# Kernel tuning notes

Hardware: AMD Instinct MI355X
Metric: run time of the kernel (lower is better)

Reference implementation:

```python
import jax, jax.numpy as jnp
import numpy as np

B, S, D, H = 2, 1024, 1024, 16
DK = D // H  # 64, per-head dim; quaternion component dim = DK // 4 = 16
NEG = -1e9


def qlinear(x, wr, wi, wj, wk, b):
    """Quaternion linear layer: Hamilton product x (x) W, per-component weights (D/4, D/4)."""
    xr, xi, xj, xk = jnp.split(x, 4, axis=-1)
    o_r = xr @ wr - xi @ wi - xj @ wj - xk @ wk
    o_i = xr @ wi + xi @ wr + xj @ wk - xk @ wj
    o_j = xr @ wj - xi @ wk + xj @ wr + xk @ wi
    o_k = xr @ wk + xi @ wj - xj @ wi + xk @ wr
    return jnp.concatenate([o_r, o_i, o_j, o_k], axis=-1) + b


def quat_scores(q, k):
    """Hamilton product q (x) k^T over chunked head dim. q,k: [B,H,S,DK]."""
    ar, ax, ay, az = jnp.split(q, 4, axis=-1)
    br, bx, by, bz = jnp.split(k, 4, axis=-1)
    mm = lambda a, b: jnp.einsum('bhsd,bhtd->bhst', a, b)
    r = mm(ar, br) - mm(ax, bx) - mm(ay, by) - mm(az, bz)
    i = mm(ar, bx) + mm(ax, br) + mm(ay, bz) - mm(az, by)
    j = mm(ar, by) - mm(ax, bz) + mm(ay, br) + mm(az, bx)
    kk = mm(ar, bz) + mm(ax, by) - mm(ay, bx) + mm(az, br)
    return r, i, j, kk


def quat_mix(sr, si, sj, sk, v):
    """Hamilton product scores (x) v (no transpose). s*: [B,H,S,S], v: [B,H,S,DK]."""
    br, bx, by, bz = jnp.split(v, 4, axis=-1)
    mm = lambda a, b: jnp.einsum('bhst,bhtd->bhsd', a, b)
    r = mm(sr, br) - mm(si, bx) - mm(sj, by) - mm(sk, bz)
    i = mm(sr, bx) + mm(si, br) + mm(sj, bz) - mm(sk, by)
    j = mm(sr, by) - mm(si, bz) + mm(sj, br) + mm(sk, bx)
    k = mm(sr, bz) + mm(si, by) - mm(sj, bx) + mm(sk, br)
    return jnp.concatenate([r, i, j, k], axis=-1)


def mha_forward(q, k, v, mask,
                wq_r, wq_i, wq_j, wq_k, bq,
                wk_r, wk_i, wk_j, wk_k, bk,
                wv_r, wv_i, wv_j, wv_k, bv,
                wo_r, wo_i, wo_j, wo_k, bo):
    bs = q.shape[0]
    def heads(x):
        return x.reshape(bs, -1, H, DK).transpose(0, 2, 1, 3)  # [B,H,S,DK]
    qh = heads(qlinear(q, wq_r, wq_i, wq_j, wq_k, bq))
    kh = heads(qlinear(k, wk_r, wk_i, wk_j, wk_k, bk))
    vh = heads(qlinear(v, wv_r, wv_i, wv_j, wv_k, bv))
    scale = 1.0 / jnp.sqrt(jnp.asarray(DK, qh.dtype))
    sr, si, sj, sk = [s * scale for s in quat_scores(qh, kh)]
    m = (mask[:, None] != 0)  # [B,1,1,S] broadcast over [B,H,S,S]
    sm = lambda s: jax.nn.softmax(jnp.where(m, s, NEG), axis=-1)
    out = quat_mix(sm(sr), sm(si), sm(sj), sm(sk), vh)  # [B,H,S,DK]
    concat = out.transpose(0, 2, 1, 3).reshape(bs, -1, D)
    return qlinear(concat, wo_r, wo_i, wo_j, wo_k, bo)


def setup_inputs() -> dict:
    key = jax.random.key(0)
    ks = jax.random.split(key, 24)
    dq = D // 4
    w_scale = 1.0 / np.sqrt(dq)
    inp = {
        'q': jax.random.normal(ks[0], (B, S, D), jnp.float32),
        'k': jax.random.normal(ks[1], (B, S, D), jnp.float32),
        'v': jax.random.normal(ks[2], (B, S, D), jnp.float32),
        'mask': jnp.ones((B, 1, S), jnp.int32),
    }
    names = ['wq_r', 'wq_i', 'wq_j', 'wq_k', 'wk_r', 'wk_i', 'wk_j', 'wk_k',
             'wv_r', 'wv_i', 'wv_j', 'wv_k', 'wo_r', 'wo_i', 'wo_j', 'wo_k']
    for n, kk in zip(names, ks[3:19]):
        inp[n] = jax.random.normal(kk, (dq, dq), jnp.float32) * w_scale
    for n, kk in zip(['bq', 'bk', 'bv', 'bo'], ks[19:23]):
        inp[n] = jax.random.normal(kk, (D,), jnp.float32) * 0.01
    return inp


def reference(q, k, v, mask,
              wq_r, wq_i, wq_j, wq_k, bq,
              wk_r, wk_i, wk_j, wk_k, bk,
              wv_r, wv_i, wv_j, wv_k, bv,
              wo_r, wo_i, wo_j, wo_k, bo):
    return mha_forward(q, k, v, mask,
                       wq_r, wq_i, wq_j, wq_k, bq,
                       wk_r, wk_i, wk_j, wk_k, bk,
                       wv_r, wv_i, wv_j, wv_k, bv,
                       wo_r, wo_i, wo_j, wo_k, bo)
```

## Files before the change

kernel.cpp:

```cpp
#include <hip/hip_runtime.h>

#define LOG2E 1.4426950408889634f
#define SC2   0.18033688011112042f

typedef short s16x8 __attribute__((ext_vector_type(8)));
typedef short s16x4 __attribute__((ext_vector_type(4)));
typedef float f32x4 __attribute__((ext_vector_type(4)));
typedef unsigned int u32x4 __attribute__((ext_vector_type(4)));

static __device__ __forceinline__ unsigned short f2bf(float f) {
  return __builtin_bit_cast(unsigned short, (__bf16)f);
}

static __device__ __forceinline__ void gload_lds16(const void* g, void* l) {
  __builtin_amdgcn_global_load_lds(
      (__attribute__((address_space(1))) void*)g,
      (__attribute__((address_space(3))) void*)l, 16, 0, 0);
}

__global__ void k_f2b(const float* __restrict__ a, const float* __restrict__ b,
                      const float* __restrict__ c, unsigned short* __restrict__ oa,
                      unsigned short* __restrict__ ob, unsigned short* __restrict__ oc) {
  const int z = blockIdx.y;
  const float* in = z == 0 ? a : z == 1 ? b : c;
  unsigned short* out = z == 0 ? oa : z == 1 ? ob : oc;
  int i = blockIdx.x * blockDim.x + threadIdx.x;
  const float4 v = ((const float4*)in)[i];
  ushort4 o;
  o.x = f2bf(v.x); o.y = f2bf(v.y); o.z = f2bf(v.z); o.w = f2bf(v.w);
  ((ushort4*)out)[i] = o;
}

struct WArgs {
  const float* w[16];
  unsigned short* dst[4];
};
__global__ void k_build_w(WArgs args) {
  __shared__ float tile[64][65];
  const int z = blockIdx.y;
  const int k0 = (blockIdx.x & 15) * 64, n0 = (blockIdx.x >> 4) * 64;
  const int a = k0 >> 8, c = n0 >> 8;
  const int   selr[16] = {0,1,2,3, 1,0,3,2, 2,3,0,1, 3,2,1,0};
  const float sgnr[16] = {1,1,1,1, -1,1,-1,1, -1,1,1,-1, -1,-1,1,1};
  const float* sp = args.w[z*4 + selr[a*4 + c]];
  const float sg = sgnr[a*4 + c];
  unsigned short* Wt = args.dst[z];
  const int k0l = k0 & 255, n0l = n0 & 255;
  const int rr = threadIdx.x >> 6, cc = threadIdx.x & 63;
#pragma unroll
  for (int p = 0; p < 16; ++p) {
    int r = p*4 + rr;
    tile[r][cc] = sp[(k0l + r)*256 + n0l + cc];
  }
  __syncthreads();
#pragma unroll
  for (int p = 0; p < 16; ++p) {
    int nn = p*4 + rr;
    Wt[(size_t)(n0 + nn)*1024 + k0 + cc] = f2bf(tile[cc][nn] * sg);
  }
}

__global__ __launch_bounds__(256, 2) void k_gemm_qkv(
    const unsigned short* __restrict__ Xq, const unsigned short* __restrict__ Xk,
    const unsigned short* __restrict__ Xv,
    const unsigned short* __restrict__ Wq, const unsigned short* __restrict__ Wk,
    const unsigned short* __restrict__ Wv,
    const float* __restrict__ bq, const float* __restrict__ bk, const float* __restrict__ bv,
    unsigned short* __restrict__ Qp, unsigned short* __restrict__ Kp,
    unsigned short* __restrict__ VpT) {
  __shared__ unsigned short As[2][128*32];
  __shared__ unsigned short Bs[2][128*32];
  const int z = blockIdx.z;
  const unsigned short* A  = z == 0 ? Xq : z == 1 ? Xk : Xv;
  const unsigned short* Bt = z == 0 ? Wq : z == 1 ? Wk : Wv;
  const float* bias        = z == 0 ? bq : z == 1 ? bk : bv;
  const int K = 1024, N = 1024;
  const int tid = threadIdx.x;
  const int lane = tid & 63, wave = tid >> 6;
  const int lo = lane & 15, hi = lane >> 4;
  const int m0 = blockIdx.x * 128, n0 = blockIdx.y * 128;
  const int wr_ = (wave >> 1) * 64, wc_ = (wave & 1) * 64;
  const int e0 = tid*8, e1 = 2048 + tid*8;
  const int r0 = e0 >> 5, c0 = e0 & 31, r1 = e1 >> 5, c1 = e1 & 31;
  f32x4 acc[4][4] = {};

  gload_lds16(A  + (size_t)(m0 + r0)*K + c0, &As[0][e0]);
  gload_lds16(Bt + (size_t)(n0 + r0)*K + c0, &Bs[0][e0]);
  gload_lds16(A  + (size_t)(m0 + r1)*K + c1, &As[0][e1]);
  gload_lds16(Bt + (size_t)(n0 + r1)*K + c1, &Bs[0][e1]);
  __syncthreads();
  int cur = 0;
  for (int k0 = 0; k0 < K; k0 += 32) {
    if (k0 + 32 < K) {
      int kn = k0 + 32;
      gload_lds16(A  + (size_t)(m0 + r0)*K + (kn + c0), &As[cur^1][e0]);
      gload_lds16(Bt + (size_t)(n0 + r0)*K + (kn + c0), &Bs[cur^1][e0]);
      gload_lds16(A  + (size_t)(m0 + r1)*K + (kn + c1), &As[cur^1][e1]);
      gload_lds16(Bt + (size_t)(n0 + r1)*K + (kn + c1), &Bs[cur^1][e1]);
    }
    s16x8 af[4], bfv[4];
#pragma unroll
    for (int mf = 0; mf < 4; ++mf)
      af[mf] = __builtin_bit_cast(s16x8, *(const u32x4*)&As[cur][(wr_ + mf*16 + lo)*32 + hi*8]);
#pragma unroll
    for (int nf = 0; nf < 4; ++nf)
      bfv[nf] = __builtin_bit_cast(s16x8, *(const u32x4*)&Bs[cur][(wc_ + nf*16 + lo)*32 + hi*8]);
#pragma unroll
    for (int mf = 0; mf < 4; ++mf)
#pragma unroll
      for (int nf = 0; nf < 4; ++nf)
        acc[mf][nf] = __builtin_amdgcn_mfma_f32_16x16x32_bf16(af[mf], bfv[nf], acc[mf][nf], 0, 0, 0);
    __syncthreads();
    cur ^= 1;
  }
  if (z < 2) {
    unsigned short* Cout = z == 0 ? Qp : Kp;
#pragma unroll
    for (int nf = 0; nf < 4; ++nf) {
      int col = n0 + wc_ + nf*16 + lo;
      float bv2 = bias[col];
#pragma unroll
      for (int mf = 0; mf < 4; ++mf)
#pragma unroll
        for (int j = 0; j < 4; ++j) {
          int row = m0 + wr_ + mf*16 + hi*4 + j;
          Cout[(size_t)row*N + col] = f2bf(acc[mf][nf][j] + bv2);
        }
    }
  } else {
#pragma unroll
    for (int nf = 0; nf < 4; ++nf) {
      int col = n0 + wc_ + nf*16 + lo;
      float bv2 = bias[col];
      int hh = col >> 6, dk = col & 63;
#pragma unroll
      for (int mf = 0; mf < 4; ++mf) {
        int row = m0 + wr_ + mf*16 + hi*4;
        int bb = row >> 10, t = row & 1023;
        s16x4 pk;
#pragma unroll
        for (int j = 0; j < 4; ++j) pk[j] = (short)f2bf(acc[mf][nf][j] + bv2);
        *(s16x4*)(VpT + ((size_t)((bb*16 + hh)*64 + dk))*1024 + t) = pk;
      }
    }
  }
}

__global__ __launch_bounds__(256, 2) void k_gemm_o(
    const unsigned short* __restrict__ A, const unsigned short* __restrict__ Bt,
    const float* __restrict__ bias, float* __restrict__ Cout) {
  __shared__ unsigned short As[2][128*32];
  __shared__ unsigned short Bs[2][128*32];
  const int K = 1024, N = 1024;
  const int tid = threadIdx.x;
  const int lane = tid & 63, wave = tid >> 6;
  const int lo = lane & 15, hi = lane >> 4;
  const int m0 = blockIdx.x * 128, n0 = blockIdx.y * 128;
  const int wr_ = (wave >> 1) * 64, wc_ = (wave & 1) * 64;
  const int e0 = tid*8, e1 = 2048 + tid*8;
  const int r0 = e0 >> 5, c0 = e0 & 31, r1 = e1 >> 5, c1 = e1 & 31;
  f32x4 acc[4][4] = {};
  gload_lds16(A  + (size_t)(m0 + r0)*K + c0, &As[0][e0]);
  gload_lds16(Bt + (size_t)(n0 + r0)*K + c0, &Bs[0][e0]);
  gload_lds16(A  + (size_t)(m0 + r1)*K + c1, &As[0][e1]);
  gload_lds16(Bt + (size_t)(n0 + r1)*K + c1, &Bs[0][e1]);
  __syncthreads();
  int cur = 0;
  for (int k0 = 0; k0 < K; k0 += 32) {
    if (k0 + 32 < K) {
      int kn = k0 + 32;
      gload_lds16(A  + (size_t)(m0 + r0)*K + (kn + c0), &As[cur^1][e0]);
      gload_lds16(Bt + (size_t)(n0 + r0)*K + (kn + c0), &Bs[cur^1][e0]);
      gload_lds16(A  + (size_t)(m0 + r1)*K + (kn + c1), &As[cur^1][e1]);
      gload_lds16(Bt + (size_t)(n0 + r1)*K + (kn + c1), &Bs[cur^1][e1]);
    }
    s16x8 af[4], bfv[4];
#pragma unroll
    for (int mf = 0; mf < 4; ++mf)
      af[mf] = __builtin_bit_cast(s16x8, *(const u32x4*)&As[cur][(wr_ + mf*16 + lo)*32 + hi*8]);
#pragma unroll
    for (int nf = 0; nf < 4; ++nf)
      bfv[nf] = __builtin_bit_cast(s16x8, *(const u32x4*)&Bs[cur][(wc_ + nf*16 + lo)*32 + hi*8]);
#pragma unroll
    for (int mf = 0; mf < 4; ++mf)
#pragma unroll
      for (int nf = 0; nf < 4; ++nf)
        acc[mf][nf] = __builtin_amdgcn_mfma_f32_16x16x32_bf16(af[mf], bfv[nf], acc[mf][nf], 0, 0, 0);
    __syncthreads();
    cur ^= 1;
  }
#pragma unroll
  for (int nf = 0; nf < 4; ++nf) {
    int col = n0 + wc_ + nf*16 + lo;
    float bv2 = bias[col];
#pragma unroll
    for (int mf = 0; mf < 4; ++mf)
#pragma unroll
      for (int j = 0; j < 4; ++j) {
        int row = m0 + wr_ + mf*16 + hi*4 + j;
        Cout[(size_t)row*N + col] = acc[mf][nf][j] + bv2;
      }
  }
}

__global__ __launch_bounds__(256, 2) void k_attn(
    const unsigned short* __restrict__ Qp, const unsigned short* __restrict__ Kp,
    const unsigned short* __restrict__ VpT, const int* __restrict__ mask,
    unsigned short* __restrict__ O) {
  __shared__ float mbias[1024];
  const int bh = blockIdx.x & 31, qb = blockIdx.x >> 5;
  const int b = bh >> 4, h = bh & 15;
  for (int t = threadIdx.x; t < 1024; t += 256)
    mbias[t] = mask[b*1024 + t] ? 0.0f : -2.0e9f;
  __syncthreads();
  const int lane = threadIdx.x & 63, wave = threadIdx.x >> 6;
  const int lo = lane & 15, hi = lane >> 4;
  const int s0 = qb*64 + wave*16;

  const int qsel[16] = {0,1,2,3, 1,0,3,2, 2,3,0,1, 3,2,1,0};
  const int qsgn[16] = {1,-1,-1,-1, 1,1,-1,1, 1,1,1,-1, 1,-1,1,1};
  const int vsgn[16] = {1,1,1,1, -1,1,-1,1, -1,1,1,-1, -1,-1,1,1};

  s16x8 qf[4][2];
  {
    const size_t qoff = ((size_t)(b*1024 + s0 + lo))*1024 + h*64;
    const int ch_hi = hi >> 1, dlo = (hi & 1) * 8;
#pragma unroll
    for (int c = 0; c < 4; ++c)
#pragma unroll
      for (int kb = 0; kb < 2; ++kb) {
        int ch = kb*2 + ch_hi;
        int p = qsel[c*4 + ch];
        u32x4 raw = *(const u32x4*)(Qp + qoff + p*16 + dlo);
        unsigned int mk = (qsgn[c*4 + ch] < 0) ? 0x80008000u : 0u;
        raw ^= mk;
        qf[c][kb] = __builtin_bit_cast(s16x8, raw);
      }
  }

  f32x4 acc[4][4] = {};
  float lsum[4] = {0.f, 0.f, 0.f, 0.f};

  const unsigned short* vtb = VpT + ((size_t)bh*64 + lo)*1024;

  for (int t0 = 0; t0 < 1024; t0 += 32) {
    const size_t koffA = ((size_t)(b*1024 + t0 + lo))*1024 + h*64;
    s16x8 kfA0 = __builtin_bit_cast(s16x8, *(const u32x4*)(Kp + koffA + hi*8));
    s16x8 kfA1 = __builtin_bit_cast(s16x8, *(const u32x4*)(Kp + koffA + 32 + hi*8));
    const size_t koffB = koffA + (size_t)16*1024;
    s16x8 kfB0 = __builtin_bit_cast(s16x8, *(const u32x4*)(Kp + koffB + hi*8));
    s16x8 kfB1 = __builtin_bit_cast(s16x8, *(const u32x4*)(Kp + koffB + 32 + hi*8));
    s16x4 vA[4], vB[4], vAn[4], vBn[4];
#pragma unroll
    for (int g = 0; g < 4; ++g) {
      vA[g] = *(const s16x4*)(vtb + (size_t)g*16*1024 + t0 + hi*4);
      vB[g] = *(const s16x4*)(vtb + (size_t)g*16*1024 + t0 + 16 + hi*4);
    }
    vAn[0] = vA[0]; vBn[0] = vB[0];
#pragma unroll
    for (int g = 1; g < 4; ++g) {
      vAn[g] = vA[g] ^ (short)0x8000;
      vBn[g] = vB[g] ^ (short)0x8000;
    }
    f32x4 mbA = *(const f32x4*)&mbias[t0 + hi*4];
    f32x4 mbB = *(const f32x4*)&mbias[t0 + 16 + hi*4];

#pragma unroll
    for (int c = 0; c < 4; ++c) {
      f32x4 sA = {0.f,0.f,0.f,0.f}, sB = {0.f,0.f,0.f,0.f};
      sA = __builtin_amdgcn_mfma_f32_16x16x32_bf16(kfA0, qf[c][0], sA, 0, 0, 0);
      sA = __builtin_amdgcn_mfma_f32_16x16x32_bf16(kfA1, qf[c][1], sA, 0, 0, 0);
      sB = __builtin_amdgcn_mfma_f32_16x16x32_bf16(kfB0, qf[c][0], sB, 0, 0, 0);
      sB = __builtin_amdgcn_mfma_f32_16x16x32_bf16(kfB1, qf[c][1], sB, 0, 0, 0);
      float p0 = __builtin_exp2f(__builtin_fmaf(sA[0], SC2, mbA[0]));
      float p1 = __builtin_exp2f(__builtin_fmaf(sA[1], SC2, mbA[1]));
      float p2 = __builtin_exp2f(__builtin_fmaf(sA[2], SC2, mbA[2]));
      float p3 = __builtin_exp2f(__builtin_fmaf(sA[3], SC2, mbA[3]));
      float p4 = __builtin_exp2f(__builtin_fmaf(sB[0], SC2, mbB[0]));
      float p5 = __builtin_exp2f(__builtin_fmaf(sB[1], SC2, mbB[1]));
      float p6 = __builtin_exp2f(__builtin_fmaf(sB[2], SC2, mbB[2]));
      float p7 = __builtin_exp2f(__builtin_fmaf(sB[3], SC2, mbB[3]));
      lsum[c] += ((p0 + p1) + (p2 + p3)) + ((p4 + p5) + (p6 + p7));
      s16x4 pfA, pfB;
      pfA[0] = (short)f2bf(p0); pfA[1] = (short)f2bf(p1);
      pfA[2] = (short)f2bf(p2); pfA[3] = (short)f2bf(p3);
      pfB[0] = (short)f2bf(p4); pfB[1] = (short)f2bf(p5);
      pfB[2] = (short)f2bf(p6); pfB[3] = (short)f2bf(p7);
#pragma unroll
      for (int g = 0; g < 4; ++g) {
        int idx = c*4 + g;
        int p = qsel[idx];
        s16x4 va = vsgn[idx] < 0 ? vAn[p] : vA[p];
        s16x4 vb = vsgn[idx] < 0 ? vBn[p] : vB[p];
        acc[c][g] = __builtin_amdgcn_mfma_f32_16x16x16bf16_1k(pfA, va, acc[c][g], 0, 0, 0);
        acc[c][g] = __builtin_amdgcn_mfma_f32_16x16x16bf16_1k(pfB, vb, acc[c][g], 0, 0, 0);
      }
    }
  }
  float rl[4];
#pragma unroll
  for (int c = 0; c < 4; ++c) {
    float l = lsum[c];
    l += __shfl_xor(l, 16);
    l += __shfl_xor(l, 32);
    rl[c] = 1.0f / l;
  }
  const size_t obase = ((size_t)(b*1024 + s0 + hi*4))*1024 + h*64;
#pragma unroll
  for (int j = 0; j < 4; ++j) {
    float r0 = __shfl(rl[0], hi*4 + j);
    float r1 = __shfl(rl[1], hi*4 + j);
    float r2 = __shfl(rl[2], hi*4 + j);
    float r3 = __shfl(rl[3], hi*4 + j);
#pragma unroll
    for (int g = 0; g < 4; ++g) {
      float o = acc[0][g][j]*r0 + acc[1][g][j]*r1 + acc[2][g][j]*r2 + acc[3][g][j]*r3;
      O[obase + (size_t)j*1024 + g*16 + lo] = f2bf(o);
    }
  }
}

extern "C" void kernel_launch(void* const* d_in, const int* in_sizes, int n_in,
                              void* d_out, int out_size, void* d_ws, size_t ws_size,
                              hipStream_t stream) {
  const float* q  = (const float*)d_in[0];
  const float* k  = (const float*)d_in[1];
  const float* v  = (const float*)d_in[2];
  const int* mask = (const int*)d_in[3];
  const float* bq = (const float*)d_in[20];
  const float* bk = (const float*)d_in[21];
  const float* bv = (const float*)d_in[22];
  const float* bo = (const float*)d_in[23];

  unsigned short* ws = (unsigned short*)d_ws;
  unsigned short* Xq = ws;
  unsigned short* Xk = Xq + 2048*1024;
  unsigned short* Xv = Xk + 2048*1024;
  unsigned short* Wq = Xv + 2048*1024;
  unsigned short* Wk = Wq + 1024*1024;
  unsigned short* Wv = Wk + 1024*1024;
  unsigned short* Wo = Wv + 1024*1024;
  unsigned short* Qp = Wo + 1024*1024;
  unsigned short* Kp = Qp + 2048*1024;
  unsigned short* VpT = Kp + 2048*1024;
  unsigned short* Ob = VpT + 2048*1024;

  k_f2b<<<dim3(2048, 3), 256, 0, stream>>>(q, k, v, Xq, Xk, Xv);

  WArgs wa;
  for (int i = 0; i < 16; ++i) wa.w[i] = (const float*)d_in[4 + i];
  wa.dst[0] = Wq; wa.dst[1] = Wk; wa.dst[2] = Wv; wa.dst[3] = Wo;
  k_build_w<<<dim3(256, 4), 256, 0, stream>>>(wa);

  k_gemm_qkv<<<dim3(16, 8, 3), 256, 0, stream>>>(Xq, Xk, Xv, Wq, Wk, Wv,
                                                 bq, bk, bv, Qp, Kp, VpT);
  k_attn<<<512, 256, 0, stream>>>(Qp, Kp, VpT, mask, Ob);
  k_gemm_o<<<dim3(16, 8), 256, 0, stream>>>(Ob, Wo, bo, (float*)d_out);
}
```

Measured before the change: 253.2 us.

## Split attention key range across two blocks and add combine kernel

Attention blocks now each process half of the key sequence, doubling the grid size, and write unnormalized bf16 partial outputs and row sums to workspace. A new combine kernel adds the two partials, normalizes by the summed row sums, and writes the bf16 output. This aims to raise GPU occupancy and parallelism. The cost is an extra launch, extra global memory traffic for the partials, and some bf16 rounding of intermediate accumulators.

```diff
diff --git a/kernel.cpp b/kernel.cpp
--- a/kernel.cpp
+++ b/kernel.cpp
@@ -10,6 +10,9 @@
 
 static __device__ __forceinline__ unsigned short f2bf(float f) {
   return __builtin_bit_cast(unsigned short, (__bf16)f);
+}
+static __device__ __forceinline__ float bf2f(unsigned short u) {
+  return __builtin_bit_cast(float, ((unsigned int)u) << 16);
 }
 
 static __device__ __forceinline__ void gload_lds16(const void* g, void* l) {
@@ -206,12 +209,12 @@
 __global__ __launch_bounds__(256, 2) void k_attn(
     const unsigned short* __restrict__ Qp, const unsigned short* __restrict__ Kp,
     const unsigned short* __restrict__ VpT, const int* __restrict__ mask,
-    unsigned short* __restrict__ O) {
-  __shared__ float mbias[1024];
-  const int bh = blockIdx.x & 31, qb = blockIdx.x >> 5;
+    unsigned short* __restrict__ Pacc, float* __restrict__ Plsum) {
+  __shared__ float mbias[512];
+  const int bh = blockIdx.x & 31, qb = (blockIdx.x >> 5) & 15, tc = blockIdx.x >> 9;
   const int b = bh >> 4, h = bh & 15;
-  for (int t = threadIdx.x; t < 1024; t += 256)
-    mbias[t] = mask[b*1024 + t] ? 0.0f : -2.0e9f;
+  for (int t = threadIdx.x; t < 512; t += 256)
+    mbias[t] = mask[b*1024 + tc*512 + t] ? 0.0f : -2.0e9f;
   __syncthreads();
   const int lane = threadIdx.x & 63, wave = threadIdx.x >> 6;
   const int lo = lane & 15, hi = lane >> 4;
@@ -242,8 +245,10 @@
   float lsum[4] = {0.f, 0.f, 0.f, 0.f};
 
   const unsigned short* vtb = VpT + ((size_t)bh*64 + lo)*1024;
-
-  for (int t0 = 0; t0 < 1024; t0 += 32) {
+  const int tbeg = tc * 512;
+
+  for (int tl = 0; tl < 512; tl += 32) {
+    const int t0 = tbeg + tl;
     const size_t koffA = ((size_t)(b*1024 + t0 + lo))*1024 + h*64;
     s16x8 kfA0 = __builtin_bit_cast(s16x8, *(const u32x4*)(Kp + koffA + hi*8));
     s16x8 kfA1 = __builtin_bit_cast(s16x8, *(const u32x4*)(Kp + koffA + 32 + hi*8));
@@ -262,8 +267,8 @@
       vAn[g] = vA[g] ^ (short)0x8000;
       vBn[g] = vB[g] ^ (short)0x8000;
     }
-    f32x4 mbA = *(const f32x4*)&mbias[t0 + hi*4];
-    f32x4 mbB = *(const f32x4*)&mbias[t0 + 16 + hi*4];
+    f32x4 mbA = *(const f32x4*)&mbias[tl + hi*4];
+    f32x4 mbB = *(const f32x4*)&mbias[tl + 16 + hi*4];
 
 #pragma unroll
     for (int c = 0; c < 4; ++c) {
@@ -297,27 +302,73 @@
       }
     }
   }
-  float rl[4];
+
+  const int b_idx = (tc*32 + bh)*16 + qb;
 #pragma unroll
   for (int c = 0; c < 4; ++c) {
     float l = lsum[c];
     l += __shfl_xor(l, 16);
     l += __shfl_xor(l, 32);
-    rl[c] = 1.0f / l;
-  }
+    if (hi == 0) Plsum[b_idx*256 + wave*64 + c*16 + lo] = l;
+  }
+  unsigned short* pb = Pacc + (size_t)b_idx*16384 + wave*4096;
+#pragma unroll
+  for (int c = 0; c < 4; ++c)
+#pragma unroll
+    for (int g = 0; g < 4; ++g) {
+      s16x4 pk;
+#pragma unroll
+      for (int j = 0; j < 4; ++j) pk[j] = (short)f2bf(acc[c][g][j]);
+      *(s16x4*)(pb + (c*4 + g)*256 + lane*4) = pk;
+    }
+}
+
+__global__ __launch_bounds__(256) void k_comb(
+    const unsigned short* __restrict__ Pacc, const float* __restrict__ Plsum,
+    unsigned short* __restrict__ O) {
+  __shared__ float lsm[2][256];
+  const int bh = blockIdx.x & 31, qb = blockIdx.x >> 5;
+  const int b = bh >> 4, h = bh & 15;
+  const int tid = threadIdx.x;
+  const int i0 = (bh*16 + qb)*256, i1 = ((32 + bh)*16 + qb)*256;
+  lsm[0][tid] = Plsum[i0 + tid];
+  lsm[1][tid] = Plsum[i1 + tid];
+  __syncthreads();
+  const int lane = tid & 63, wave = tid >> 6;
+  const int lo = lane & 15, hi = lane >> 4;
+  const size_t a0 = ((size_t)(bh*16 + qb))*16384 + wave*4096;
+  const size_t a1 = ((size_t)((32 + bh)*16 + qb))*16384 + wave*4096;
+  float rl[4][4];
+#pragma unroll
+  for (int c = 0; c < 4; ++c)
+#pragma unroll
+    for (int j = 0; j < 4; ++j) {
+      int r = wave*64 + c*16 + hi*4 + j;
+      rl[c][j] = 1.0f / (lsm[0][r] + lsm[1][r]);
+    }
+  f32x4 av[4][4];
+#pragma unroll
+  for (int c = 0; c < 4; ++c)
+#pragma unroll
+    for (int g = 0; g < 4; ++g) {
+      s16x4 x0 = *(const s16x4*)(Pacc + a0 + (c*4 + g)*256 + lane*4);
+      s16x4 x1 = *(const s16x4*)(Pacc + a1 + (c*4 + g)*256 + lane*4);
+      f32x4 s;
+#pragma unroll
+      for (int j = 0; j < 4; ++j)
+        s[j] = bf2f((unsigned short)x0[j]) + bf2f((unsigned short)x1[j]);
+      av[c][g] = s;
+    }
+  const int s0 = qb*64 + wave*16;
   const size_t obase = ((size_t)(b*1024 + s0 + hi*4))*1024 + h*64;
 #pragma unroll
-  for (int j = 0; j < 4; ++j) {
-    float r0 = __shfl(rl[0], hi*4 + j);
-    float r1 = __shfl(rl[1], hi*4 + j);
-    float r2 = __shfl(rl[2], hi*4 + j);
-    float r3 = __shfl(rl[3], hi*4 + j);
+  for (int j = 0; j < 4; ++j)
 #pragma unroll
     for (int g = 0; g < 4; ++g) {
-      float o = acc[0][g][j]*r0 + acc[1][g][j]*r1 + acc[2][g][j]*r2 + acc[3][g][j]*r3;
+      float o = av[0][g][j]*rl[0][j] + av[1][g][j]*rl[1][j]
+              + av[2][g][j]*rl[2][j] + av[3][g][j]*rl[3][j];
       O[obase + (size_t)j*1024 + g*16 + lo] = f2bf(o);
     }
-  }
 }
 
 extern "C" void kernel_launch(void* const* d_in, const int* in_sizes, int n_in,
@@ -332,18 +383,21 @@
   const float* bv = (const float*)d_in[22];
   const float* bo = (const float*)d_in[23];
 
+  const size_t M1 = 1024*1024;
   unsigned short* ws = (unsigned short*)d_ws;
   unsigned short* Xq = ws;
-  unsigned short* Xk = Xq + 2048*1024;
-  unsigned short* Xv = Xk + 2048*1024;
-  unsigned short* Wq = Xv + 2048*1024;
-  unsigned short* Wk = Wq + 1024*1024;
-  unsigned short* Wv = Wk + 1024*1024;
-  unsigned short* Wo = Wv + 1024*1024;
-  unsigned short* Qp = Wo + 1024*1024;
-  unsigned short* Kp = Qp + 2048*1024;
-  unsigned short* VpT = Kp + 2048*1024;
-  unsigned short* Ob = VpT + 2048*1024;
+  unsigned short* Xk = Xq + 2*M1;
+  unsigned short* Xv = Xk + 2*M1;
+  unsigned short* Wq = Xv + 2*M1;
+  unsigned short* Wk = Wq + M1;
+  unsigned short* Wv = Wk + M1;
+  unsigned short* Wo = Wv + M1;
+  unsigned short* Qp = Wo + M1;
+  unsigned short* Kp = Qp + 2*M1;
+  unsigned short* VpT = Kp + 2*M1;
+  unsigned short* Ob = VpT + 2*M1;
+  unsigned short* Pacc = Ob + 2*M1;
+  float* Plsum = (float*)(Pacc + 16*M1);
 
   k_f2b<<<dim3(2048, 3), 256, 0, stream>>>(q, k, v, Xq, Xk, Xv);
 
@@ -354,6 +408,7 @@
 
   k_gemm_qkv<<<dim3(16, 8, 3), 256, 0, stream>>>(Xq, Xk, Xv, Wq, Wk, Wv,
                                                  bq, bk, bv, Qp, Kp, VpT);
-  k_attn<<<512, 256, 0, stream>>>(Qp, Kp, VpT, mask, Ob);
+  k_attn<<<1024, 256, 0, stream>>>(Qp, Kp, VpT, mask, Pacc, Plsum);
+  k_comb<<<512, 256, 0, stream>>>(Pacc, Plsum, Ob);
   k_gemm_o<<<dim3(16, 8), 256, 0, stream>>>(Ob, Wo, bo, (float*)d_out);
 }
```

Result: slower. 267.9 us (+5.8%).

## Merge prep kernels and shrink GEMM N-tile to 64 for more blocks

Applied to the files above, without the earlier changes.

Merges the fp32-to-bf16 activation conversion and the quaternion weight-build kernels into a single launch, removing one kernel launch and its gap. Both projection GEMMs move from 128x128 to 128x64 output tiles with launch bounds of 3 blocks per CU. This doubles the grid, so the output GEMM gets 256 blocks instead of 128 and fills the 256 CUs better. The trade-off is less operand reuse per block, so A tiles are reloaded from memory twice as often.

```diff
diff --git a/kernel.cpp b/kernel.cpp
--- a/kernel.cpp
+++ b/kernel.cpp
@@ -18,49 +18,51 @@
       (__attribute__((address_space(3))) void*)l, 16, 0, 0);
 }
 
-__global__ void k_f2b(const float* __restrict__ a, const float* __restrict__ b,
-                      const float* __restrict__ c, unsigned short* __restrict__ oa,
-                      unsigned short* __restrict__ ob, unsigned short* __restrict__ oc) {
-  const int z = blockIdx.y;
-  const float* in = z == 0 ? a : z == 1 ? b : c;
-  unsigned short* out = z == 0 ? oa : z == 1 ? ob : oc;
-  int i = blockIdx.x * blockDim.x + threadIdx.x;
-  const float4 v = ((const float4*)in)[i];
-  ushort4 o;
-  o.x = f2bf(v.x); o.y = f2bf(v.y); o.z = f2bf(v.z); o.w = f2bf(v.w);
-  ((ushort4*)out)[i] = o;
-}
-
-struct WArgs {
+struct PrepArgs {
+  const float* q; const float* k; const float* v;
+  unsigned short* xq; unsigned short* xk; unsigned short* xv;
   const float* w[16];
   unsigned short* dst[4];
 };
-__global__ void k_build_w(WArgs args) {
+__global__ void k_prep(PrepArgs pa) {
   __shared__ float tile[64][65];
-  const int z = blockIdx.y;
-  const int k0 = (blockIdx.x & 15) * 64, n0 = (blockIdx.x >> 4) * 64;
-  const int a = k0 >> 8, c = n0 >> 8;
-  const int   selr[16] = {0,1,2,3, 1,0,3,2, 2,3,0,1, 3,2,1,0};
-  const float sgnr[16] = {1,1,1,1, -1,1,-1,1, -1,1,1,-1, -1,-1,1,1};
-  const float* sp = args.w[z*4 + selr[a*4 + c]];
-  const float sg = sgnr[a*4 + c];
-  unsigned short* Wt = args.dst[z];
-  const int k0l = k0 & 255, n0l = n0 & 255;
-  const int rr = threadIdx.x >> 6, cc = threadIdx.x & 63;
-#pragma unroll
-  for (int p = 0; p < 16; ++p) {
-    int r = p*4 + rr;
-    tile[r][cc] = sp[(k0l + r)*256 + n0l + cc];
-  }
-  __syncthreads();
-#pragma unroll
-  for (int p = 0; p < 16; ++p) {
-    int nn = p*4 + rr;
-    Wt[(size_t)(n0 + nn)*1024 + k0 + cc] = f2bf(tile[cc][nn] * sg);
-  }
-}
-
-__global__ __launch_bounds__(256, 2) void k_gemm_qkv(
+  const int blk = blockIdx.x;
+  if (blk < 6144) {
+    const int z = blk >> 11;
+    const int i = ((blk & 2047) << 8) + threadIdx.x;
+    const float* in = z == 0 ? pa.q : z == 1 ? pa.k : pa.v;
+    unsigned short* out = z == 0 ? pa.xq : z == 1 ? pa.xk : pa.xv;
+    const float4 v = ((const float4*)in)[i];
+    ushort4 o;
+    o.x = f2bf(v.x); o.y = f2bf(v.y); o.z = f2bf(v.z); o.w = f2bf(v.w);
+    ((ushort4*)out)[i] = o;
+  } else {
+    const int blk2 = blk - 6144;
+    const int z = blk2 >> 8, bx = blk2 & 255;
+    const int k0 = (bx & 15) * 64, n0 = (bx >> 4) * 64;
+    const int a = k0 >> 8, c = n0 >> 8;
+    const int   selr[16] = {0,1,2,3, 1,0,3,2, 2,3,0,1, 3,2,1,0};
+    const float sgnr[16] = {1,1,1,1, -1,1,-1,1, -1,1,1,-1, -1,-1,1,1};
+    const float* sp = pa.w[z*4 + selr[a*4 + c]];
+    const float sg = sgnr[a*4 + c];
+    unsigned short* Wt = pa.dst[z];
+    const int k0l = k0 & 255, n0l = n0 & 255;
+    const int rr = threadIdx.x >> 6, cc = threadIdx.x & 63;
+#pragma unroll
+    for (int p = 0; p < 16; ++p) {
+      int r = p*4 + rr;
+      tile[r][cc] = sp[(k0l + r)*256 + n0l + cc];
+    }
+    __syncthreads();
+#pragma unroll
+    for (int p = 0; p < 16; ++p) {
+      int nn = p*4 + rr;
+      Wt[(size_t)(n0 + nn)*1024 + k0 + cc] = f2bf(tile[cc][nn] * sg);
+    }
+  }
+}
+
+__global__ __launch_bounds__(256, 3) void k_gemm_qkv(
     const unsigned short* __restrict__ Xq, const unsigned short* __restrict__ Xk,
     const unsigned short* __restrict__ Xv,
     const unsigned short* __restrict__ Wq, const unsigned short* __restrict__ Wk,
@@ -69,7 +71,7 @@
     unsigned short* __restrict__ Qp, unsigned short* __restrict__ Kp,
     unsigned short* __restrict__ VpT) {
   __shared__ unsigned short As[2][128*32];
-  __shared__ unsigned short Bs[2][128*32];
+  __shared__ unsigned short Bs[2][64*32];
   const int z = blockIdx.z;
   const unsigned short* A  = z == 0 ? Xq : z == 1 ? Xk : Xv;
   const unsigned short* Bt = z == 0 ? Wq : z == 1 ? Wk : Wv;
@@ -78,37 +80,35 @@
   const int tid = threadIdx.x;
   const int lane = tid & 63, wave = tid >> 6;
   const int lo = lane & 15, hi = lane >> 4;
-  const int m0 = blockIdx.x * 128, n0 = blockIdx.y * 128;
-  const int wr_ = (wave >> 1) * 64, wc_ = (wave & 1) * 64;
+  const int m0 = blockIdx.x * 128, n0 = blockIdx.y * 64;
+  const int wr_ = (wave & 1) * 64, wc_ = (wave >> 1) * 32;
   const int e0 = tid*8, e1 = 2048 + tid*8;
   const int r0 = e0 >> 5, c0 = e0 & 31, r1 = e1 >> 5, c1 = e1 & 31;
-  f32x4 acc[4][4] = {};
+  f32x4 acc[4][2] = {};
 
   gload_lds16(A  + (size_t)(m0 + r0)*K + c0, &As[0][e0]);
+  gload_lds16(A  + (size_t)(m0 + r1)*K + c1, &As[0][e1]);
   gload_lds16(Bt + (size_t)(n0 + r0)*K + c0, &Bs[0][e0]);
-  gload_lds16(A  + (size_t)(m0 + r1)*K + c1, &As[0][e1]);
-  gload_lds16(Bt + (size_t)(n0 + r1)*K + c1, &Bs[0][e1]);
   __syncthreads();
   int cur = 0;
   for (int k0 = 0; k0 < K; k0 += 32) {
     if (k0 + 32 < K) {
       int kn = k0 + 32;
       gload_lds16(A  + (size_t)(m0 + r0)*K + (kn + c0), &As[cur^1][e0]);
+      gload_lds16(A  + (size_t)(m0 + r1)*K + (kn + c1), &As[cur^1][e1]);
       gload_lds16(Bt + (size_t)(n0 + r0)*K + (kn + c0), &Bs[cur^1][e0]);
-      gload_lds16(A  + (size_t)(m0 + r1)*K + (kn + c1), &As[cur^1][e1]);
-      gload_lds16(Bt + (size_t)(n0 + r1)*K + (kn + c1), &Bs[cur^1][e1]);
-    }
-    s16x8 af[4], bfv[4];
+    }
+    s16x8 af[4], bfv[2];
 #pragma unroll
     for (int mf = 0; mf < 4; ++mf)
       af[mf] = __builtin_bit_cast(s16x8, *(const u32x4*)&As[cur][(wr_ + mf*16 + lo)*32 + hi*8]);
 #pragma unroll
-    for (int nf = 0; nf < 4; ++nf)
+    for (int nf = 0; nf < 2; ++nf)
       bfv[nf] = __builtin_bit_cast(s16x8, *(const u32x4*)&Bs[cur][(wc_ + nf*16 + lo)*32 + hi*8]);
 #pragma unroll
     for (int mf = 0; mf < 4; ++mf)
 #pragma unroll
-      for (int nf = 0; nf < 4; ++nf)
+      for (int nf = 0; nf < 2; ++nf)
         acc[mf][nf] = __builtin_amdgcn_mfma_f32_16x16x32_bf16(af[mf], bfv[nf], acc[mf][nf], 0, 0, 0);
     __syncthreads();
     cur ^= 1;
@@ -116,7 +116,7 @@
   if (z < 2) {
     unsigned short* Cout = z == 0 ? Qp : Kp;
 #pragma unroll
-    for (int nf = 0; nf < 4; ++nf) {
+    for (int nf = 0; nf < 2; ++nf) {
       int col = n0 + wc_ + nf*16 + lo;
       float bv2 = bias[col];
 #pragma unroll
@@ -129,7 +129,7 @@
     }
   } else {
 #pragma unroll
-    for (int nf = 0; nf < 4; ++nf) {
+    for (int nf = 0; nf < 2; ++nf) {
       int col = n0 + wc_ + nf*16 + lo;
       float bv2 = bias[col];
       int hh = col >> 6, dk = col & 63;
@@ -146,51 +146,49 @@
   }
 }
 
-__global__ __launch_bounds__(256, 2) void k_gemm_o(
+__global__ __launch_bounds__(256, 3) void k_gemm_o(
     const unsigned short* __restrict__ A, const unsigned short* __restrict__ Bt,
     const float* __restrict__ bias, float* __restrict__ Cout) {
   __shared__ unsigned short As[2][128*32];
-  __shared__ unsigned short Bs[2][128*32];
+  __shared__ unsigned short Bs[2][64*32];
   const int K = 1024, N = 1024;
   const int tid = threadIdx.x;
   const int lane = tid & 63, wave = tid >> 6;
   const int lo = lane & 15, hi = lane >> 4;
-  const int m0 = blockIdx.x * 128, n0 = blockIdx.y * 128;
-  const int wr_ = (wave >> 1) * 64, wc_ = (wave & 1) * 64;
+  const int m0 = blockIdx.x * 128, n0 = blockIdx.y * 64;
+  const int wr_ = (wave & 1) * 64, wc_ = (wave >> 1) * 32;
   const int e0 = tid*8, e1 = 2048 + tid*8;
   const int r0 = e0 >> 5, c0 = e0 & 31, r1 = e1 >> 5, c1 = e1 & 31;
-  f32x4 acc[4][4] = {};
+  f32x4 acc[4][2] = {};
   gload_lds16(A  + (size_t)(m0 + r0)*K + c0, &As[0][e0]);
+  gload_lds16(A  + (size_t)(m0 + r1)*K + c1, &As[0][e1]);
   gload_lds16(Bt + (size_t)(n0 + r0)*K + c0, &Bs[0][e0]);
-  gload_lds16(A  + (size_t)(m0 + r1)*K + c1, &As[0][e1]);
-  gload_lds16(Bt + (size_t)(n0 + r1)*K + c1, &Bs[0][e1]);
   __syncthreads();
   int cur = 0;
   for (int k0 = 0; k0 < K; k0 += 32) {
     if (k0 + 32 < K) {
       int kn = k0 + 32;
       gload_lds16(A  + (size_t)(m0 + r0)*K + (kn + c0), &As[cur^1][e0]);
+      gload_lds16(A  + (size_t)(m0 + r1)*K + (kn + c1), &As[cur^1][e1]);
       gload_lds16(Bt + (size_t)(n0 + r0)*K + (kn + c0), &Bs[cur^1][e0]);
-      gload_lds16(A  + (size_t)(m0 + r1)*K + (kn + c1), &As[cur^1][e1]);
-      gload_lds16(Bt + (size_t)(n0 + r1)*K + (kn + c1), &Bs[cur^1][e1]);
-    }
-    s16x8 af[4], bfv[4];
+    }
+    s16x8 af[4], bfv[2];
 #pragma unroll
     for (int mf = 0; mf < 4; ++mf)
       af[mf] = __builtin_bit_cast(s16x8, *(const u32x4*)&As[cur][(wr_ + mf*16 + lo)*32 + hi*8]);
 #pragma unroll
-    for (int nf = 0; nf < 4; ++nf)
+    for (int nf = 0; nf < 2; ++nf)
       bfv[nf] = __builtin_bit_cast(s16x8, *(const u32x4*)&Bs[cur][(wc_ + nf*16 + lo)*32 + hi*8]);
 #pragma unroll
     for (int mf = 0; mf < 4; ++mf)
 #pragma unroll
-      for (int nf = 0; nf < 4; ++nf)
+      for (int nf = 0; nf < 2; ++nf)
         acc[mf][nf] = __builtin_amdgcn_mfma_f32_16x16x32_bf16(af[mf], bfv[nf], acc[mf][nf], 0, 0, 0);
     __syncthreads();
     cur ^= 1;
   }
 #pragma unroll
-  for (int nf = 0; nf < 4; ++nf) {
+  for (int nf = 0; nf < 2; ++nf) {
     int col = n0 + wc_ + nf*16 + lo;
     float bv2 = bias[col];
 #pragma unroll
@@ -332,28 +330,29 @@
   const float* bv = (const float*)d_in[22];
   const float* bo = (const float*)d_in[23];
 
+  const size_t M1 = 1024*1024;
   unsigned short* ws = (unsigned short*)d_ws;
   unsigned short* Xq = ws;
-  unsigned short* Xk = Xq + 2048*1024;
-  unsigned short* Xv = Xk + 2048*1024;
-  unsigned short* Wq = Xv + 2048*1024;
-  unsigned short* Wk = Wq + 1024*1024;
-  unsigned short* Wv = Wk + 1024*1024;
-  unsigned short* Wo = Wv + 1024*1024;
-  unsigned short* Qp = Wo + 1024*1024;
-  unsigned short* Kp = Qp + 2048*1024;
-  unsigned short* VpT = Kp + 2048*1024;
-  unsigned short* Ob = VpT + 2048*1024;
-
-  k_f2b<<<dim3(2048, 3), 256, 0, stream>>>(q, k, v, Xq, Xk, Xv);
-
-  WArgs wa;
-  for (int i = 0; i < 16; ++i) wa.w[i] = (const float*)d_in[4 + i];
-  wa.dst[0] = Wq; wa.dst[1] = Wk; wa.dst[2] = Wv; wa.dst[3] = Wo;
-  k_build_w<<<dim3(256, 4), 256, 0, stream>>>(wa);
-
-  k_gemm_qkv<<<dim3(16, 8, 3), 256, 0, stream>>>(Xq, Xk, Xv, Wq, Wk, Wv,
-                                                 bq, bk, bv, Qp, Kp, VpT);
+  unsigned short* Xk = Xq + 2*M1;
+  unsigned short* Xv = Xk + 2*M1;
+  unsigned short* Wq = Xv + 2*M1;
+  unsigned short* Wk = Wq + M1;
+  unsigned short* Wv = Wk + M1;
+  unsigned short* Wo = Wv + M1;
+  unsigned short* Qp = Wo + M1;
+  unsigned short* Kp = Qp + 2*M1;
+  unsigned short* VpT = Kp + 2*M1;
+  unsigned short* Ob = VpT + 2*M1;
+
+  PrepArgs pa;
+  pa.q = q; pa.k = k; pa.v = v;
+  pa.xq = Xq; pa.xk = Xk; pa.xv = Xv;
+  for (int i = 0; i < 16; ++i) pa.w[i] = (const float*)d_in[4 + i];
+  pa.dst[0] = Wq; pa.dst[1] = Wk; pa.dst[2] = Wv; pa.dst[3] = Wo;
+  k_prep<<<7168, 256, 0, stream>>>(pa);
+
+  k_gemm_qkv<<<dim3(16, 16, 3), 256, 0, stream>>>(Xq, Xk, Xv, Wq, Wk, Wv,
+                                                  bq, bk, bv, Qp, Kp, VpT);
   k_attn<<<512, 256, 0, stream>>>(Qp, Kp, VpT, mask, Ob);
-  k_gemm_o<<<dim3(16, 8), 256, 0, stream>>>(Ob, Wo, bo, (float*)d_out);
-}
+  k_gemm_o<<<dim3(16, 16), 256, 0, stream>>>(Ob, Wo, bo, (float*)d_out);
+}
```

Result: slower. 259.9 us (+2.6%).
